# Kernel optimization log

Hardware: AMD Instinct MI355X
Metric: run time of the kernel (lower is better)

The kernel has to match this reference:

```python
import jax, jax.numpy as jnp
import numpy as np

B, S, D_TEXT, MAXF = 2, 1024, 384, 5
D_MODEL, N_HEADS, D_FF, L = 768, 12, 3072, 4
HEAD_DIM = D_MODEL // N_HEADS
EPS = 1e-6
NEG = -1e9


def _rms(x, g):
    return x * jax.lax.rsqrt(jnp.mean(x * x, axis=-1, keepdims=True) + EPS) * g


def _attn(x, w, mask):
    # w: [4, d, d] = (wq, wk, wv, wo); mask: [b, s, s] bool (True = attend)
    b, s, d = x.shape

    def proj(W):
        return jnp.einsum('bsd,de->bse', x, W).reshape(b, s, N_HEADS, HEAD_DIM).transpose(0, 2, 1, 3)

    q, k, v = proj(w[0]), proj(w[1]), proj(w[2])
    scale = jnp.asarray(1.0 / np.sqrt(HEAD_DIM), x.dtype)
    scores = jnp.einsum('bhqe,bhke->bhqk', q, k) * scale
    scores = jnp.where(mask[:, None], scores, NEG)
    p = jax.nn.softmax(scores, axis=-1)
    o = jnp.einsum('bhqk,bhke->bhqe', p, v).transpose(0, 2, 1, 3).reshape(b, s, d)
    return jnp.einsum('bsd,de->bse', o, w[3])


def _forward(number_values, datetime_values, boolean_values, text_values, column_name_values,
             W_cn, b_cn, W_num, b_num, W_text, b_text, W_dt, b_dt, W_bool, b_bool,
             g_cn, g_num, g_text, g_dt, g_bool, mask_emb,
             blk_norms, blk_attn, blk_up, blk_gate, blk_down,
             g_out, Wd_num, bd_num, Wd_dt, bd_dt, Wd_bool, bd_bool, Wd_text, bd_text,
             node_indices, table_name_indices, column_name_indices,
             f2p_neighbor_indices, semantic_types, masks, is_padding):
    valid = ~is_padding
    pv = valid[:, :, None] & valid[:, None, :]  # [b,s,s]
    eye = jnp.eye(S, dtype=bool)[None]
    same_node = node_indices[:, :, None] == node_indices[:, None, :]
    col_mask = ((column_name_indices[:, :, None] == column_name_indices[:, None, :])
                & (table_name_indices[:, :, None] == table_name_indices[:, None, :]) & pv) | eye
    feat_mask = (same_node & pv) | eye
    # kv node is one of q's f2p neighbors
    nei = (f2p_neighbor_indices[:, :, :, None] == node_indices[:, None, None, :]).any(axis=2)
    nei_mask = ((nei | same_node) & pv) | eye
    full_mask = pv | eye

    # per-semantic-type value encoders (Linear + RMSNorm)
    cn = _rms(column_name_values @ W_cn + b_cn, g_cn)
    num_e = _rms(number_values @ W_num + b_num, g_num)
    text_e = _rms(text_values @ W_text + b_text, g_text)
    dt_e = _rms(datetime_values @ W_dt + b_dt, g_dt)
    bool_e = _rms(boolean_values @ W_bool + b_bool, g_bool)
    st = semantic_types[..., None]
    val = jnp.where(st == 0, num_e, jnp.where(st == 1, text_e, jnp.where(st == 2, dt_e, bool_e)))
    # masked cells get the learned mask embedding for their semantic type
    val = jnp.where(masks[..., None], mask_emb[semantic_types], val)
    x = val + cn

    for i in range(L):
        nw, aw = blk_norms[i], blk_attn[i]
        x = x + _attn(_rms(x, nw[0]), aw[0], col_mask)
        x = x + _attn(_rms(x, nw[1]), aw[1], feat_mask)
        x = x + _attn(_rms(x, nw[2]), aw[2], nei_mask)
        x = x + _attn(_rms(x, nw[3]), aw[3], full_mask)
        h = _rms(x, nw[4])
        x = x + (jax.nn.silu(h @ blk_gate[i]) * (h @ blk_up[i])) @ blk_down[i]

    h = _rms(x, g_out)
    return (h @ Wd_num + bd_num, h @ Wd_dt + bd_dt, h @ Wd_bool + bd_bool, h @ Wd_text + bd_text)


def setup_inputs() -> dict:
    key = jax.random.key(0)
    ks = iter(jax.random.split(key, 64))

    def nrm(shape, scale=0.02):
        return jax.random.normal(next(ks), shape, jnp.float32) * scale

    inp = {}
    inp['number_values'] = jax.random.normal(next(ks), (B, S, 1), jnp.float32)
    inp['datetime_values'] = jax.random.normal(next(ks), (B, S, 1), jnp.float32)
    inp['boolean_values'] = jax.random.normal(next(ks), (B, S, 1), jnp.float32)
    inp['text_values'] = jax.random.normal(next(ks), (B, S, D_TEXT), jnp.float32)
    inp['column_name_values'] = jax.random.normal(next(ks), (B, S, D_TEXT), jnp.float32)
    inp['W_cn'] = nrm((D_TEXT, D_MODEL)); inp['b_cn'] = jnp.zeros((D_MODEL,), jnp.float32)
    inp['W_num'] = nrm((1, D_MODEL)); inp['b_num'] = jnp.zeros((D_MODEL,), jnp.float32)
    inp['W_text'] = nrm((D_TEXT, D_MODEL)); inp['b_text'] = jnp.zeros((D_MODEL,), jnp.float32)
    inp['W_dt'] = nrm((1, D_MODEL)); inp['b_dt'] = jnp.zeros((D_MODEL,), jnp.float32)
    inp['W_bool'] = nrm((1, D_MODEL)); inp['b_bool'] = jnp.zeros((D_MODEL,), jnp.float32)
    for n in ('g_cn', 'g_num', 'g_text', 'g_dt', 'g_bool'):
        inp[n] = jnp.ones((D_MODEL,), jnp.float32)
    inp['mask_emb'] = jax.random.normal(next(ks), (4, D_MODEL), jnp.float32)
    inp['blk_norms'] = jnp.ones((L, 5, D_MODEL), jnp.float32)
    inp['blk_attn'] = nrm((L, 4, 4, D_MODEL, D_MODEL))
    inp['blk_up'] = nrm((L, D_MODEL, D_FF))
    inp['blk_gate'] = nrm((L, D_MODEL, D_FF))
    inp['blk_down'] = nrm((L, D_FF, D_MODEL))
    inp['g_out'] = jnp.ones((D_MODEL,), jnp.float32)
    inp['Wd_num'] = nrm((D_MODEL, 1)); inp['bd_num'] = jnp.zeros((1,), jnp.float32)
    inp['Wd_dt'] = nrm((D_MODEL, 1)); inp['bd_dt'] = jnp.zeros((1,), jnp.float32)
    inp['Wd_bool'] = nrm((D_MODEL, 1)); inp['bd_bool'] = jnp.zeros((1,), jnp.float32)
    inp['Wd_text'] = nrm((D_MODEL, D_TEXT)); inp['bd_text'] = jnp.zeros((D_TEXT,), jnp.float32)
    inp['node_indices'] = jax.random.randint(next(ks), (B, S), 0, 128)
    inp['table_name_indices'] = jax.random.randint(next(ks), (B, S), 0, 8)
    inp['column_name_indices'] = jax.random.randint(next(ks), (B, S), 0, 32)
    inp['f2p_neighbor_indices'] = jax.random.randint(next(ks), (B, S, MAXF), 0, 128)
    inp['semantic_types'] = jax.random.randint(next(ks), (B, S), 0, 4)
    inp['masks'] = jax.random.bernoulli(next(ks), 0.15, (B, S))
    inp['is_padding'] = jnp.zeros((B, S), bool)
    return inp


def reference(number_values, datetime_values, boolean_values, text_values, column_name_values,
              W_cn, b_cn, W_num, b_num, W_text, b_text, W_dt, b_dt, W_bool, b_bool,
              g_cn, g_num, g_text, g_dt, g_bool, mask_emb,
              blk_norms, blk_attn, blk_up, blk_gate, blk_down,
              g_out, Wd_num, bd_num, Wd_dt, bd_dt, Wd_bool, bd_bool, Wd_text, bd_text,
              node_indices, table_name_indices, column_name_indices,
              f2p_neighbor_indices, semantic_types, masks, is_padding):
    return _forward(number_values, datetime_values, boolean_values, text_values, column_name_values,
                    W_cn, b_cn, W_num, b_num, W_text, b_text, W_dt, b_dt, W_bool, b_bool,
                    g_cn, g_num, g_text, g_dt, g_bool, mask_emb,
                    blk_norms, blk_attn, blk_up, blk_gate, blk_down,
                    g_out, Wd_num, bd_num, Wd_dt, bd_dt, Wd_bool, bd_bool, Wd_text, bd_text,
                    node_indices, table_name_indices, column_name_indices,
                    f2p_neighbor_indices, semantic_types, masks, is_padding)
```

## Files before the change

kernel.cpp:

```cpp
#include <hip/hip_runtime.h>
#include <hip/hip_bf16.h>
#include <cmath>
#include <stdint.h>


#define BB 2
#define SS 1024
#define DT 384
#define DM 768
#define NH 12
#define DH 64
#define DFF 3072
#define NL 4
#define NROW (BB*SS)
#define EPSF 1e-6f
#define QSC 0.1803368801111244f

typedef unsigned short u16;
typedef unsigned char u8;
typedef unsigned int u32;
typedef __attribute__((ext_vector_type(8))) short s16x8;
typedef __attribute__((ext_vector_type(4))) float f32x4;

__device__ __forceinline__ u16 f2bu(float f){
    u32 x = __float_as_uint(f);
    u32 r = (x + 0x7fffu + ((x>>16)&1u)) >> 16;
    return (u16)r;
}
__device__ __forceinline__ u32 pk2(float lo, float hi){
    return (u32)f2bu(lo) | ((u32)f2bu(hi)<<16);
}
__device__ __forceinline__ int swz(int row, int c){
    return (row<<6) + (((((c>>3) ^ row) & 7))<<3) + (c&7);
}
__device__ __forceinline__ float rsum16(float v){
    v += __shfl_xor(v,1); v += __shfl_xor(v,2);
    v += __shfl_xor(v,4); v += __shfl_xor(v,8);
    return v;
}
#define SBAR() __builtin_amdgcn_sched_barrier(0)
#define GLDS(src,dst) __builtin_amdgcn_global_load_lds((const __attribute__((address_space(1))) u32*)(src), (__attribute__((address_space(3))) u32*)(dst), 16, 0, 0)
#define GLDS4(src,dst) __builtin_amdgcn_global_load_lds((const __attribute__((address_space(1))) u32*)(src), (__attribute__((address_space(3))) u32*)(dst), 4, 0, 0)

__global__ void zero_f(float* __restrict__ p, int n){
    int i = blockIdx.x*256 + threadIdx.x;
    if (i<n) p[i]=0.f;
}

__device__ void norm_bool_body(const void* __restrict__ src, u8* __restrict__ dst, int n)
{
    __shared__ int fl[4];
    if (threadIdx.x<4) fl[threadIdx.x]=0;
    __syncthreads();
    const u32* wsrc = (const u32*)src;
    const int nw = n/4;
    int any=0, nb=0, hi=0, lo=0;
    for (int i=threadIdx.x;i<nw;i+=blockDim.x){
        u32 v=wsrc[i];
        if (!v) continue;
        any=1;
        #pragma unroll
        for (int b=0;b<4;b++){
            u32 by=(v>>(8*b))&0xffu;
            if (by>1u) nb=1;
            if (by==1u && b!=0) hi=1;
        }
        if ((v&0xffffu)==0x3f80u) lo=1;
    }
    if (any) atomicOr(&fl[0],1);
    if (nb)  atomicOr(&fl[1],1);
    if (hi)  atomicOr(&fl[2],1);
    if (lo)  atomicOr(&fl[3],1);
    __syncthreads();
    int c;
    if (!fl[0]) c=0;
    else if (!fl[1]) c = fl[2] ? 2 : 1;
    else if (fl[3]) c = 3;
    else c = 1;
    for (int i=threadIdx.x;i<n;i+=blockDim.x){
        u8 v;
        if (c==0)      v=0;
        else if (c==1) v = (((const u32*)src)[i]!=0u);
        else if (c==2) v = (((const u8*)src)[i]!=0u);
        else           v = (((const u16*)src)[i]!=0u);
        dst[i]=v;
    }
}
__global__ void norm_bool2(const void* s0, u8* d0, const void* s1, u8* d1, int n)
{
    if (blockIdx.x==0) norm_bool_body(s0,d0,n);
    else               norm_bool_body(s1,d1,n);
}

__global__ void pack_meta(const int* __restrict__ node, const int* __restrict__ colx,
                          const int* __restrict__ tbl, const u8* __restrict__ pad,
                          u32* __restrict__ pm, int n)
{
    int i = blockIdx.x*256 + threadIdx.x;
    if (i<n)
        pm[i] = (u32)(node[i]&0xff) | ((u32)(colx[i]&0xff)<<8) | ((u32)(tbl[i]&0xff)<<16) | ((u32)(pad[i]&1)<<24);
}

__global__ __launch_bounds__(256) void mask4_kernel(const u32* __restrict__ pm, const int* __restrict__ f2p,
                                                    u8* __restrict__ m4)
{
    const int b = blockIdx.y, kg = blockIdx.x;
    const int t = threadIdx.x;
    __shared__ u32 qm[1024];
    __shared__ int qf[1024*5];
    for (int i=t;i<1024;i+=256) qm[i] = pm[b*SS+i];
    for (int i=t;i<5*1024;i+=256) qf[i] = f2p[b*SS*5 + i];
    __syncthreads();
    const int q0 = t*4;
    u32 qmv[4]; int qn[4]; int qfv[4][5];
    #pragma unroll
    for (int j=0;j<4;j++){
        qmv[j]=qm[q0+j]; qn[j]=(int)(qmv[j]&0xffu);
        #pragma unroll
        for (int f=0;f<5;f++) qfv[j][f]=qf[(q0+j)*5+f];
    }
    for (int kk=0;kk<16;kk++){
        const int k = kg*16+kk;
        const u32 km = qm[k];
        const int kn = (int)(km&0xffu);
        u32 outw=0;
        #pragma unroll
        for (int j=0;j<4;j++){
            const u32 qmw = qmv[j];
            const bool pv = (((qmw|km)>>24)&1u)==0u;
            u32 by=0;
            if ((((qmw^km)&0x00ffff00u)==0u) && pv) by|=1;
            if ((((qmw^km)&0xffu)==0u) && pv) by|=2;
            bool nei = (qfv[j][0]==kn)||(qfv[j][1]==kn)||(qfv[j][2]==kn)||(qfv[j][3]==kn)||(qfv[j][4]==kn)
                       ||(qn[j]==kn);
            if (nei && pv) by|=4;
            if (pv) by|=8;
            if ((q0+j)==k) by=15;
            outw |= by<<(8*j);
        }
        ((u32*)(m4 + ((size_t)b<<20) + ((size_t)k<<10)))[t] = outw;
    }
}

__global__ __launch_bounds__(256) void transpose_cvt2(const float* __restrict__ src, u16* __restrict__ dst,
                                                      int K, int N, size_t dz,
                                                      const float* __restrict__ gbase, int gmode)
{
    const int z = blockIdx.z;
    src += (size_t)z*K*N;
    dst += (size_t)z*dz;
    const float* g = nullptr;
    if (gmode==1){ int m = z&3; if (m<3) g = gbase + (size_t)((z>>4)*5 + ((z>>2)&3))*768; }
    else if (gmode==2){ g = gbase + (size_t)z*5*768; }
    const int n0 = blockIdx.x*32, k0 = blockIdx.y*64;
    __shared__ float t[64][33];
    const int tid = threadIdx.x;
    const int kr = tid>>3, n4 = (tid&7)*4;
    #pragma unroll
    for (int p=0;p<2;p++){
        const int k = p*32 + kr;
        float gk = g ? g[k0+k] : 1.f;
        float4 v = *(const float4*)(src + (size_t)(k0+k)*N + n0 + n4);
        t[k][n4]=v.x*gk; t[k][n4+1]=v.y*gk; t[k][n4+2]=v.z*gk; t[k][n4+3]=v.w*gk;
    }
    __syncthreads();
    const int n = tid>>3, ks = (tid&7)*8;
    const int ng = n0 + n;
    uint4 o;
    u32* op = (u32*)&o;
    #pragma unroll
    for (int i=0;i<4;i++)
        op[i] = pk2(t[ks+2*i][n], t[ks+2*i+1][n]);
    *(uint4*)&dst[(((size_t)(ng>>7)*(K>>6) + (k0>>6))<<13) + ((ng&127)<<6) + ks] = o;
}

__global__ __launch_bounds__(256) void cvt_tiled2(const float* __restrict__ s0, u16* __restrict__ d0,
                                                  const float* __restrict__ s1, u16* __restrict__ d1, int K)
{
    const float* src = blockIdx.y ? s1 : s0;
    u16* dst = blockIdx.y ? d1 : d0;
    const int gid = blockIdx.x*256 + threadIdx.x;
    const int base = gid*8;
    const int row = base / K, col = base - row*K;
    float4 a = *(const float4*)(src + base);
    float4 b = *(const float4*)(src + base + 4);
    uint4 o;
    o.x = pk2(a.x,a.y); o.y = pk2(a.z,a.w);
    o.z = pk2(b.x,b.y); o.w = pk2(b.z,b.w);
    *(uint4*)&dst[(((size_t)(row>>7)*(K>>6) + (col>>6))<<13) + ((row&127)<<6) + (col&63)] = o;
}

__device__ __forceinline__ void stage3(const u16* aT, const u16* bT, int cb, int brow,
                                       u16* la, u16* lb, int w, int l)
{
    #pragma unroll
    for (int p=0;p<2;p++){
        const int q = p*256 + w*64 + l;
        const int row = q>>2, u = q&3;
        const int so = row*64 + cb + (((u ^ ((row>>1)&3))&3)<<3);
        GLDS(aT+so, la + p*2048 + w*512);
    }
    {
        const int q = w*64 + l;
        const int row = q>>2, u = q&3;
        const int so = (brow+row)*64 + cb + (((u ^ ((row>>1)&3))&3)<<3);
        GLDS(bT+so, lb + w*512);
    }
}

__global__ __launch_bounds__(256,4) void gemm_t(
    const u16* __restrict__ At, const u16* __restrict__ Bt,
    int K, int AMS, u16* __restrict__ qk16, u16* __restrict__ vt16,
    const float* __restrict__ rs_in)
{
    __shared__ u16 lds[3][6144];
    const int tid = threadIdx.x;
    const int lane = tid & 63, w = tid >> 6;
    const int cg = lane >> 4, cl = lane & 15;
    const int NT = K >> 5;
    const int n0 = blockIdx.x*64;
    const int brow = n0 & 64;
    const size_t bNb = (size_t)(n0>>7)*(K>>6);

    const u16* aB = At + ((size_t)blockIdx.y * AMS << 13);
    const u16* bB = Bt + (bNb << 13);

    f32x4 acc[2][4];
    #pragma unroll
    for (int i=0;i<2;i++)
        #pragma unroll
        for (int j=0;j<4;j++) acc[i][j] = (f32x4){0.f,0.f,0.f,0.f};

    stage3(aB, bB, 0, brow, &lds[0][0], &lds[0][4096], w, lane);

    for (int kt=0; kt<NT; kt++){
        const int buf = kt % 3;
        if (kt+1 < NT){
            const int k1 = kt+1;
            stage3(aB + ((size_t)(k1>>1)<<13), bB + ((size_t)(k1>>1)<<13),
                   (k1&1)<<5, brow, &lds[k1%3][0], &lds[k1%3][4096], w, lane);
            asm volatile("s_waitcnt vmcnt(3)" ::: "memory");
        } else {
            asm volatile("s_waitcnt vmcnt(0)" ::: "memory");
        }
        SBAR(); __builtin_amdgcn_s_barrier(); SBAR();
        s16x8 af[2], bf[4];
        #pragma unroll
        for (int mt=0;mt<2;mt++){
            const int ra = w*32 + mt*16 + cl;
            af[mt] = *(const s16x8*)&lds[buf][ra*32 + (((cg ^ ((ra>>1)&3))&3)<<3)];
        }
        #pragma unroll
        for (int nt=0;nt<4;nt++){
            const int rb = nt*16 + cl;
            bf[nt] = *(const s16x8*)&lds[buf][4096 + rb*32 + (((cg ^ ((rb>>1)&3))&3)<<3)];
        }
        #pragma unroll
        for (int mt=0;mt<2;mt++)
            #pragma unroll
            for (int nt=0;nt<4;nt++)
                acc[mt][nt] = __builtin_amdgcn_mfma_f32_16x16x32_bf16(af[mt], bf[nt], acc[mt][nt], 0,0,0);
    }

    const int m0 = blockIdx.y*128;
    #pragma unroll
    for (int mt=0;mt<2;mt++){
        const int grow0 = m0 + w*32 + mt*16 + cg*4;
        float rr[4];
        #pragma unroll
        for (int j=0;j<4;j++) rr[j] = rsqrtf(rs_in[grow0+j]*(1.f/768.f) + EPSF);
        #pragma unroll
        for (int nt=0;nt<4;nt++){
            const int col = n0 + nt*16 + cl;
            if (col < 768){
                #pragma unroll
                for (int j=0;j<4;j++)
                    qk16[(size_t)(grow0+j)*1536 + col] = f2bu(acc[mt][nt][j]*rr[j]*QSC);
            } else if (col < 1536){
                #pragma unroll
                for (int j=0;j<4;j++)
                    qk16[(size_t)(grow0+j)*1536 + col] = f2bu(acc[mt][nt][j]*rr[j]);
            } else {
                const int b = grow0>>10, s0 = grow0&1023;
                const int dhg = col - 1536;
                uint2 o;
                o.x = pk2(acc[mt][nt][0]*rr[0], acc[mt][nt][1]*rr[1]);
                o.y = pk2(acc[mt][nt][2]*rr[2], acc[mt][nt][3]*rr[3]);
                *(uint2*)(vt16 + ((size_t)(b*768 + dhg)<<10) + s0) = o;
            }
        }
    }
}

__global__ __launch_bounds__(256,3) void gemm_gu(
    const u16* __restrict__ At, const u16* __restrict__ Bg, const u16* __restrict__ Bu,
    const float* __restrict__ rs_in, u16* __restrict__ o16)
{
    __shared__ u16 lds[3][8192];
    const int tid = threadIdx.x;
    const int lane = tid & 63, w = tid >> 6;
    const int cg = lane >> 4, cl = lane & 15;
    const int NT = 24;
    const int n0 = blockIdx.x*64;
    const int brow = n0 & 64;
    const size_t bNb = (size_t)(n0>>7)*12;

    const u16* aB = At + ((size_t)blockIdx.y * 12 << 13);
    const u16* gB = Bg + (bNb << 13);
    const u16* uB = Bu + (bNb << 13);

    f32x4 accg[2][4], accu[2][4];
    #pragma unroll
    for (int i=0;i<2;i++)
        #pragma unroll
        for (int j=0;j<4;j++){ accg[i][j] = (f32x4){0.f,0.f,0.f,0.f}; accu[i][j] = (f32x4){0.f,0.f,0.f,0.f}; }

    #define STAGE_GU(kt2, cb, buf) { \
        const u16* a_ = aB + ((size_t)(kt2)<<13); \
        const u16* g_ = gB + ((size_t)(kt2)<<13); \
        const u16* u_ = uB + ((size_t)(kt2)<<13); \
        _Pragma("unroll") \
        for (int p=0;p<2;p++){ \
            const int q = p*256 + w*64 + lane; \
            const int row = q>>2, uu = q&3; \
            const int so = row*64 + (cb) + (((uu ^ ((row>>1)&3))&3)<<3); \
            GLDS(a_+so, &lds[buf][0] + p*2048 + w*512); \
        } \
        { \
            const int q = w*64 + lane; \
            const int row = q>>2, uu = q&3; \
            const int so = (brow+row)*64 + (cb) + (((uu ^ ((row>>1)&3))&3)<<3); \
            GLDS(g_+so, &lds[buf][4096] + w*512); \
            GLDS(u_+so, &lds[buf][6144] + w*512); \
        } }

    STAGE_GU(0, 0, 0);

    for (int kt=0; kt<NT; kt++){
        const int buf = kt % 3;
        if (kt+1 < NT){
            const int k1 = kt+1;
            STAGE_GU(k1>>1, (k1&1)<<5, k1%3);
            asm volatile("s_waitcnt vmcnt(4)" ::: "memory");
        } else {
            asm volatile("s_waitcnt vmcnt(0)" ::: "memory");
        }
        SBAR(); __builtin_amdgcn_s_barrier(); SBAR();
        s16x8 af[2], bg[4], bu[4];
        #pragma unroll
        for (int mt=0;mt<2;mt++){
            const int ra = w*32 + mt*16 + cl;
            af[mt] = *(const s16x8*)&lds[buf][ra*32 + (((cg ^ ((ra>>1)&3))&3)<<3)];
        }
        #pragma unroll
        for (int nt=0;nt<4;nt++){
            const int rb = nt*16 + cl;
            const int sw = (((cg ^ ((rb>>1)&3))&3)<<3);
            bg[nt] = *(const s16x8*)&lds[buf][4096 + rb*32 + sw];
            bu[nt] = *(const s16x8*)&lds[buf][6144 + rb*32 + sw];
        }
        #pragma unroll
        for (int mt=0;mt<2;mt++)
            #pragma unroll
            for (int nt=0;nt<4;nt++){
                accg[mt][nt] = __builtin_amdgcn_mfma_f32_16x16x32_bf16(af[mt], bg[nt], accg[mt][nt], 0,0,0);
                accu[mt][nt] = __builtin_amdgcn_mfma_f32_16x16x32_bf16(af[mt], bu[nt], accu[mt][nt], 0,0,0);
            }
    }

    const int m0 = blockIdx.y*128;
    #pragma unroll
    for (int mt=0;mt<2;mt++){
        const int grow0 = m0 + w*32 + mt*16 + cg*4;
        float rr[4];
        #pragma unroll
        for (int j=0;j<4;j++) rr[j] = rsqrtf(rs_in[grow0+j]*(1.f/768.f) + EPSF);
        #pragma unroll
        for (int nt=0;nt<4;nt++){
            const int col = n0 + nt*16 + cl;
            const size_t tb = (((size_t)(grow0>>7)*48 + (col>>6))<<13) + (col&63);
            #pragma unroll
            for (int j=0;j<4;j++){
                float g = accg[mt][nt][j]*rr[j];
                float u = accu[mt][nt][j]*rr[j];
                float s = g/(1.f+__expf(-g))*u;
                o16[tb + (((grow0+j)&127)<<6)] = f2bu(s);
            }
        }
    }
}

__device__ __forceinline__ void stage64(const u16* aT, int arow, const u16* bT, int brow, int cb,
                                        u16* la, u16* lb, int w, int l)
{
    const int q = w*64 + l;
    const int row = q>>2, u = q&3;
    const int sw = (((u ^ ((row>>1)&3))&3)<<3);
    GLDS(aT + (arow+row)*64 + cb + sw, la + w*512);
    GLDS(bT + (brow+row)*64 + cb + sw, lb + w*512);
}

__global__ __launch_bounds__(256,6) void gemm_t64(
    const u16* __restrict__ At, const u16* __restrict__ Bt, float* __restrict__ C,
    int N, int K, int AMS, int flags, const float* __restrict__ bias,
    u16* __restrict__ o16, float* __restrict__ rs_out)
{
    __shared__ u16 lds[3][4096];
    const int tid = threadIdx.x;
    const int lane = tid & 63, w = tid >> 6;
    const int cg = lane >> 4, cl = lane & 15;
    const int NT = K >> 5;
    const int n0 = blockIdx.x*64;
    const int m0 = blockIdx.y*64;
    const int brow = n0 & 64, arow = m0 & 64;

    const u16* aB = At + ((size_t)(m0>>7) * AMS << 13);
    const u16* bB = Bt + ((size_t)(n0>>7) * (K>>6) << 13);

    f32x4 acc[4];
    #pragma unroll
    for (int j=0;j<4;j++) acc[j] = (f32x4){0.f,0.f,0.f,0.f};

    stage64(aB, arow, bB, brow, 0, &lds[0][0], &lds[0][2048], w, lane);

    for (int kt=0; kt<NT; kt++){
        const int buf = kt % 3;
        if (kt+1 < NT){
            const int k1 = kt+1;
            stage64(aB + ((size_t)(k1>>1)<<13), arow, bB + ((size_t)(k1>>1)<<13), brow,
                    (k1&1)<<5, &lds[k1%3][0], &lds[k1%3][2048], w, lane);
            asm volatile("s_waitcnt vmcnt(2)" ::: "memory");
        } else {
            asm volatile("s_waitcnt vmcnt(0)" ::: "memory");
        }
        SBAR(); __builtin_amdgcn_s_barrier(); SBAR();
        const int ra = w*16 + cl;
        s16x8 af = *(const s16x8*)&lds[buf][ra*32 + (((cg ^ ((ra>>1)&3))&3)<<3)];
        s16x8 bf[4];
        #pragma unroll
        for (int nt=0;nt<4;nt++){
            const int rb = nt*16 + cl;
            bf[nt] = *(const s16x8*)&lds[buf][2048 + rb*32 + (((cg ^ ((rb>>1)&3))&3)<<3)];
        }
        #pragma unroll
        for (int nt=0;nt<4;nt++)
            acc[nt] = __builtin_amdgcn_mfma_f32_16x16x32_bf16(af, bf[nt], acc[nt], 0,0,0);
    }

    const int grow0 = m0 + w*16 + cg*4;
    const bool do_acc = (flags&1), do_bias = (flags&2);
    float tmp[4][4];
    #pragma unroll
    for (int nt=0;nt<4;nt++){
        const int col = n0 + nt*16 + cl;
        float bv = do_bias ? bias[col] : 0.f;
        #pragma unroll
        for (int j=0;j<4;j++){
            float v = acc[nt][j] + bv;
            float* cp = C + (size_t)(grow0+j)*N + col;
            if (do_acc) v += *cp;
            *cp = v;
            tmp[nt][j] = v;
        }
    }
    if (o16){
        #pragma unroll
        for (int nt=0;nt<4;nt++){
            const int col = n0 + nt*16 + cl;
            const size_t tb = (((size_t)(grow0>>7)*12 + (col>>6))<<13) + (col&63);
            #pragma unroll
            for (int j=0;j<4;j++)
                o16[tb + (((grow0+j)&127)<<6)] = f2bu(tmp[nt][j]);
        }
    }
    if (rs_out){
        #pragma unroll
        for (int j=0;j<4;j++){
            float s = tmp[0][j]*tmp[0][j] + tmp[1][j]*tmp[1][j]
                    + tmp[2][j]*tmp[2][j] + tmp[3][j]*tmp[3][j];
            s = rsum16(s);
            if (cl==0) atomicAdd(rs_out + grow0 + j, s);
        }
    }
}

__global__ __launch_bounds__(256,3) void attn_mfma3(
    const u16* __restrict__ qk16, const u16* __restrict__ vt16,
    const u8* __restrict__ m4, int mt,
    u16* __restrict__ ob16)
{
    const int bh = blockIdx.y;
    const int b = bh / NH, h = bh % NH;
    const int q0 = blockIdx.x * 64;
    const int tid = threadIdx.x;
    const int w = tid>>6, lane = tid&63, cg = lane>>4, cl = lane&15;
    const int srow = lane>>3;
    const int sseg = (lane&7) ^ srow;
    const int mk = lane>>4, mq = lane&15;

    __shared__ u16 Ks[2][4096], Vt[2][4096], Ps[4096];
    __shared__ u32 Ms[2][1024];

    s16x8 qa0, qa1;
    {
        const u16* qrow = qk16 + (size_t)(b*SS+q0 + w*16 + cl)*1536 + h*64;
        qa0 = *(const s16x8*)(qrow + cg*8);
        qa1 = *(const s16x8*)(qrow + 32 + cg*8);
        asm volatile("" :: "v"(*(const f32x4*)&qa0), "v"(*(const f32x4*)&qa1));
    }

    const u16* kbase = qk16 + (size_t)(b*SS)*1536 + 768 + h*64;
    const u16* vbase = vt16 + ((size_t)(b*768 + h*64)<<10);
    const u8*  mbase = m4 + ((size_t)b<<20) + q0;

    #pragma unroll
    for (int p=0;p<2;p++){
        const int row = p*32 + w*8 + srow;
        GLDS(kbase + (size_t)row*1536 + sseg*8, Ks[0] + p*2048 + w*512);
        GLDS(vbase + ((size_t)row<<10) + sseg*8, Vt[0] + p*2048 + w*512);
    }
    #pragma unroll
    for (int i=0;i<4;i++){
        const int key = w*16 + i*4 + mk;
        GLDS4(mbase + ((size_t)key<<10) + mq*4, (u8*)Ms[0] + w*1024 + i*256);
    }

    f32x4 o[4];
    #pragma unroll
    for (int nt=0;nt<4;nt++) o[nt] = (f32x4){0.f,0.f,0.f,0.f};
    float lsum[4] = {0.f,0.f,0.f,0.f};

    for (int kc=0;kc<16;kc++){
        const int buf = kc & 1;
        if (kc < 15){
            const int kn0 = kc*64 + 64;
            #pragma unroll
            for (int p=0;p<2;p++){
                const int row = p*32 + w*8 + srow;
                GLDS(kbase + (size_t)(kn0+row)*1536 + sseg*8, Ks[buf^1] + p*2048 + w*512);
                GLDS(vbase + ((size_t)row<<10) + kn0 + sseg*8, Vt[buf^1] + p*2048 + w*512);
            }
            #pragma unroll
            for (int i=0;i<4;i++){
                const int key = kn0 + w*16 + i*4 + mk;
                GLDS4(mbase + ((size_t)key<<10) + mq*4, (u8*)Ms[buf^1] + w*1024 + i*256);
            }
            asm volatile("s_waitcnt vmcnt(8)" ::: "memory");
        } else {
            asm volatile("s_waitcnt vmcnt(0)" ::: "memory");
        }
        SBAR(); __builtin_amdgcn_s_barrier(); SBAR();

        f32x4 sc[4];
        #pragma unroll
        for (int nt=0;nt<4;nt++) sc[nt] = (f32x4){0.f,0.f,0.f,0.f};
        __builtin_amdgcn_s_setprio(1);
        #pragma unroll
        for (int nt=0;nt<4;nt++){
            s16x8 kb0 = *(const s16x8*)&Ks[buf][swz(nt*16+cl, cg*8)];
            sc[nt] = __builtin_amdgcn_mfma_f32_16x16x32_bf16(qa0, kb0, sc[nt], 0,0,0);
        }
        #pragma unroll
        for (int nt=0;nt<4;nt++){
            s16x8 kb1 = *(const s16x8*)&Ks[buf][swz(nt*16+cl, 32+cg*8)];
            sc[nt] = __builtin_amdgcn_mfma_f32_16x16x32_bf16(qa1, kb1, sc[nt], 0,0,0);
        }
        __builtin_amdgcn_s_setprio(0);

        float pP[4][4];
        #pragma unroll
        for (int nt=0;nt<4;nt++){
            const u32 w4 = Ms[buf][(nt*16+cl)*16 + w*4 + cg];
            #pragma unroll
            for (int j=0;j<4;j++){
                float pe = exp2f(fminf(sc[nt][j], 100.f));
                pe = ((w4 >> (8*j + mt)) & 1u) ? pe : 0.f;
                pP[nt][j] = pe;
                lsum[j] += pe;
            }
        }

        #pragma unroll
        for (int nt=0;nt<4;nt++)
            #pragma unroll
            for (int j=0;j<4;j++)
                Ps[swz(w*16+cg*4+j, nt*16+cl)] = f2bu(pP[nt][j]);

        __builtin_amdgcn_s_setprio(1);
        #pragma unroll
        for (int ks=0;ks<2;ks++){
            s16x8 pa = *(const s16x8*)&Ps[swz(w*16+cl, ks*32+cg*8)];
            #pragma unroll
            for (int nt=0;nt<4;nt++){
                s16x8 vb = *(const s16x8*)&Vt[buf][swz(nt*16+cl, ks*32+cg*8)];
                o[nt] = __builtin_amdgcn_mfma_f32_16x16x32_bf16(pa, vb, o[nt], 0,0,0);
            }
        }
        __builtin_amdgcn_s_setprio(0);
        SBAR(); __builtin_amdgcn_s_barrier(); SBAR();
    }

    #pragma unroll
    for (int j=0;j<4;j++){
        const float inv = 1.f/rsum16(lsum[j]);
        const int row = b*SS + q0 + w*16 + cg*4 + j;
        const size_t rb = ((size_t)(row>>7)*12 + h)*8192 + ((row&127)<<6);
        #pragma unroll
        for (int nt=0;nt<4;nt++)
            ob16[rb + nt*16 + cl] = f2bu(o[nt][j]*inv);
    }
}

__global__ __launch_bounds__(256) void fuse_encode(
    const float* __restrict__ cnbuf, const float* __restrict__ textbuf,
    const float* __restrict__ numv, const float* __restrict__ dtv, const float* __restrict__ boolv,
    const float* __restrict__ Wnum, const float* __restrict__ bnum,
    const float* __restrict__ Wdt, const float* __restrict__ bdt,
    const float* __restrict__ Wbool, const float* __restrict__ bbool,
    const float* __restrict__ gcn, const float* __restrict__ gnum, const float* __restrict__ gtext,
    const float* __restrict__ gdt, const float* __restrict__ gbool,
    const float* __restrict__ memb, const int* __restrict__ stypes, const u8* __restrict__ masks,
    float* __restrict__ x, u16* __restrict__ xt16, float* __restrict__ rs0)
{
    const int row = blockIdx.x;
    const int t = threadIdx.x;
    __shared__ float red[256];

    float cn3[3]; float ss=0.f;
    #pragma unroll
    for (int j=0;j<3;j++){
        cn3[j] = cnbuf[(size_t)row*DM + t + j*256];
        ss += cn3[j]*cn3[j];
    }
    red[t]=ss; __syncthreads();
    for (int s=128;s>0;s>>=1){ if(t<s) red[t]+=red[t+s]; __syncthreads(); }
    {
        float r = rsqrtf(red[0]/(float)DM + EPSF);
        #pragma unroll
        for (int j=0;j<3;j++) cn3[j] *= r*gcn[t+j*256];
    }
    __syncthreads();

    const int st = stypes[row];
    float val[3]; ss=0.f;
    if (st==1){
        #pragma unroll
        for (int j=0;j<3;j++){
            val[j] = textbuf[(size_t)row*DM + t + j*256];
            ss += val[j]*val[j];
        }
    } else {
        const float* Wp = (st==0)?Wnum:((st==2)?Wdt:Wbool);
        const float* bp = (st==0)?bnum:((st==2)?bdt:bbool);
        const float* vp = (st==0)?numv:((st==2)?dtv:boolv);
        float v = vp[row];
        #pragma unroll
        for (int j=0;j<3;j++){
            int e=t+j*256;
            val[j] = v*Wp[e] + bp[e];
            ss += val[j]*val[j];
        }
    }
    red[t]=ss; __syncthreads();
    for (int s=128;s>0;s>>=1){ if(t<s) red[t]+=red[t+s]; __syncthreads(); }
    const float* gp = (st==0)?gnum:((st==1)?gtext:((st==2)?gdt:gbool));
    float r2 = rsqrtf(red[0]/(float)DM + EPSF);
    bool mk = masks[row]!=0;
    float xv[3]; float sx=0.f;
    #pragma unroll
    for (int j=0;j<3;j++){
        int e=t+j*256;
        float vv = val[j]*r2*gp[e];
        if (mk) vv = memb[st*DM+e];
        xv[j] = vv + cn3[j];
        x[(size_t)row*DM+e] = xv[j];
        sx += xv[j]*xv[j];
    }
    __syncthreads();
    red[t]=sx; __syncthreads();
    for (int s=128;s>0;s>>=1){ if(t<s) red[t]+=red[t+s]; __syncthreads(); }
    if (t==0) rs0[row] = red[0];
    const size_t mb = (size_t)(row>>7)*12;
    const int rr = (row&127)<<6;
    #pragma unroll
    for (int j=0;j<3;j++){
        const int c = t + j*256;
        xt16[((mb + (c>>6))<<13) + rr + (c&63)] = f2bu(xv[j]);
    }
}

__global__ __launch_bounds__(256) void decode2(
    const float* __restrict__ x, const float* __restrict__ gout,
    const float* __restrict__ Wn, const float* __restrict__ bn,
    const float* __restrict__ Wd, const float* __restrict__ bd,
    const float* __restrict__ Wb, const float* __restrict__ bb,
    float* __restrict__ out, u16* __restrict__ h16)
{
    const int row = blockIdx.x;
    const int t = threadIdx.x;
    __shared__ float h[DM];
    __shared__ float red[256];
    const float* xr = x + (size_t)row*DM;
    float v0=xr[t], v1=xr[t+256], v2=xr[t+512];
    red[t]=v0*v0+v1*v1+v2*v2; __syncthreads();
    for (int s=128;s>0;s>>=1){ if(t<s) red[t]+=red[t+s]; __syncthreads(); }
    float r = rsqrtf(red[0]/(float)DM + EPSF);
    float h0 = v0*r*gout[t], h1 = v1*r*gout[t+256], h2 = v2*r*gout[t+512];
    h[t]=h0; h[t+256]=h1; h[t+512]=h2;
    const size_t mb = (size_t)(row>>7)*12;
    const int rr = (row&127)<<6;
    #pragma unroll
    for (int j=0;j<3;j++){
        const int c = t + j*256;
        const float v = (j==0?h0:(j==1?h1:h2));
        h16[((mb + (c>>6))<<13) + rr + (c&63)] = f2bu(v);
    }
    __syncthreads();

    float pn=0.f,pd=0.f,pb=0.f;
    for (int k=t;k<DM;k+=256){ float hv=h[k]; pn+=hv*Wn[k]; pd+=hv*Wd[k]; pb+=hv*Wb[k]; }
    red[t]=pn; __syncthreads();
    for (int s=128;s>0;s>>=1){ if(t<s) red[t]+=red[t+s]; __syncthreads(); }
    float tn=red[0]; __syncthreads();
    red[t]=pd; __syncthreads();
    for (int s=128;s>0;s>>=1){ if(t<s) red[t]+=red[t+s]; __syncthreads(); }
    float td=red[0]; __syncthreads();
    red[t]=pb; __syncthreads();
    for (int s=128;s>0;s>>=1){ if(t<s) red[t]+=red[t+s]; __syncthreads(); }
    float tb=red[0];
    if (t==0){
        out[row]          = tn + bn[0];
        out[NROW + row]   = td + bd[0];
        out[2*NROW + row] = tb + bb[0];
    }
}

extern "C" void kernel_launch(void* const* d_in, const int* in_sizes, int n_in,
                              void* d_out, int out_size, void* d_ws, size_t ws_size,
                              hipStream_t stream)
{
    const float* numv   = (const float*)d_in[0];
    const float* dtval  = (const float*)d_in[1];
    const float* boolv  = (const float*)d_in[2];
    const float* textv  = (const float*)d_in[3];
    const float* cnamev = (const float*)d_in[4];
    const float* Wcn=(const float*)d_in[5];  const float* bcn=(const float*)d_in[6];
    const float* Wnum=(const float*)d_in[7]; const float* bnum=(const float*)d_in[8];
    const float* Wtext=(const float*)d_in[9];const float* btext=(const float*)d_in[10];
    const float* Wdt=(const float*)d_in[11]; const float* bdt=(const float*)d_in[12];
    const float* Wbool=(const float*)d_in[13];const float* bbool=(const float*)d_in[14];
    const float* gcn=(const float*)d_in[15]; const float* gnum=(const float*)d_in[16];
    const float* gtext=(const float*)d_in[17];const float* gdt=(const float*)d_in[18];
    const float* gbool=(const float*)d_in[19];
    const float* memb=(const float*)d_in[20];
    const float* norms_all=(const float*)d_in[21];
    const float* attw_all=(const float*)d_in[22];
    const float* up_all=(const float*)d_in[23];
    const float* gate_all=(const float*)d_in[24];
    const float* down_all=(const float*)d_in[25];
    const float* gout=(const float*)d_in[26];
    const float* Wdn=(const float*)d_in[27]; const float* bdn=(const float*)d_in[28];
    const float* Wdd=(const float*)d_in[29]; const float* bdd=(const float*)d_in[30];
    const float* Wdb=(const float*)d_in[31]; const float* bdb=(const float*)d_in[32];
    const float* Wdtx=(const float*)d_in[33];const float* bdtx=(const float*)d_in[34];
    const int* node=(const int*)d_in[35];
    const int* tbl =(const int*)d_in[36];
    const int* colx=(const int*)d_in[37];
    const int* f2p =(const int*)d_in[38];
    const int* styp=(const int*)d_in[39];

    const size_t SA = (size_t)768*768;
    const size_t SG = (size_t)768*3072;
    const size_t SC = (size_t)384*768;
    const size_t NX = (size_t)NROW*DM;

    u8* base = (u8*)d_ws;
    float* x  = (float*)base;
    u16* xt16 = (u16*)(base + 6291456);
    u16* ob16 = (u16*)(base + 9437184);
    u16* qk16 = (u16*)(base + 12582912);
    u16* vt16 = (u16*)(base + 18874368);
    u16* gu16 = (u16*)(base + 22020096);
    u16* wA   = (u16*)(base + 47185920);
    u16* wGU  = wA + 64*SA;
    u16* wD   = wGU + 8*SG;
    u16* wCN  = wD + 4*SG;
    u16* wTX  = wCN + SC;
    u16* wDX  = wTX + SC;
    u8* nmask = (u8*)(wDX + SC);
    u8* npad  = nmask + NROW;
    u32* pmeta = (u32*)(npad + NROW + 64);
    float* rsbuf = (float*)(pmeta + NROW);
    u8* m4 = (u8*)(rsbuf + 21*2048);

    u16* cnT16   = qk16;
    u16* textT16 = vt16;
    float* cnbuf   = (float*)gu16;
    float* textbuf = cnbuf + NX;

    float* out = (float*)d_out;

    zero_f<<<(21*2048)/256,256,0,stream>>>(rsbuf, 21*2048);
    norm_bool2<<<2,256,0,stream>>>(d_in[40], nmask, d_in[41], npad, NROW);
    pack_meta<<<NROW/256,256,0,stream>>>(node, colx, tbl, npad, pmeta, NROW);
    mask4_kernel<<<dim3(64,2),256,0,stream>>>(pmeta, f2p, m4);

    transpose_cvt2<<<dim3(24,12,64),256,0,stream>>>(attw_all, wA, 768, 768, SA, norms_all, 1);
    transpose_cvt2<<<dim3(96,12,4),256,0,stream>>>(gate_all, wGU,      768, 3072, 2*SG, norms_all + 4*768, 2);
    transpose_cvt2<<<dim3(96,12,4),256,0,stream>>>(up_all,   wGU + SG, 768, 3072, 2*SG, norms_all + 4*768, 2);
    transpose_cvt2<<<dim3(24,48,4),256,0,stream>>>(down_all, wD, 3072, 768, SG, nullptr, 0);
    transpose_cvt2<<<dim3(24,6,1),256,0,stream>>>(Wcn,   wCN, 384, 768, 0, nullptr, 0);
    transpose_cvt2<<<dim3(24,6,1),256,0,stream>>>(Wtext, wTX, 384, 768, 0, nullptr, 0);
    transpose_cvt2<<<dim3(12,12,1),256,0,stream>>>(Wdtx, wDX, 768, 384, 0, nullptr, 0);

    cvt_tiled2<<<dim3(384,2),256,0,stream>>>(cnamev, cnT16, textv, textT16, 384);
    gemm_t64<<<dim3(12,32),256,0,stream>>>(cnT16,   wCN, cnbuf,   768, 384, 6, 2, bcn,   nullptr, nullptr);
    gemm_t64<<<dim3(12,32),256,0,stream>>>(textT16, wTX, textbuf, 768, 384, 6, 2, btext, nullptr, nullptr);
    fuse_encode<<<NROW,256,0,stream>>>(cnbuf, textbuf, numv, dtval, boolv,
        Wnum,bnum,Wdt,bdt,Wbool,bbool, gcn,gnum,gtext,gdt,gbool,
        memb, styp, nmask, x, xt16, rsbuf);

    const dim3 ga(SS/64, BB*NH);
    for (int l=0; l<NL; l++){
        for (int a=0; a<4; a++){
            const int slot = l*5 + a;
            const u16* wqkv = wA + (size_t)((l*4+a)*4)*SA;
            gemm_t<<<dim3(36,16),256,0,stream>>>(xt16, wqkv, 768, 12, qk16, vt16,
                rsbuf + (size_t)slot*2048);
            attn_mfma3<<<ga,256,0,stream>>>(qk16, vt16, m4, a, ob16);
            gemm_t64<<<dim3(12,32),256,0,stream>>>(ob16, wqkv + 3*SA, x, 768, 768, 12, 1, nullptr,
                xt16, rsbuf + (size_t)(slot+1)*2048);
        }
        gemm_gu<<<dim3(48,16),256,0,stream>>>(xt16, wGU + (size_t)l*2*SG, wGU + (size_t)l*2*SG + SG,
            rsbuf + (size_t)(l*5+4)*2048, gu16);
        gemm_t64<<<dim3(12,32),256,0,stream>>>(gu16, wD + (size_t)l*SG, x, 768, 3072, 48, 1, nullptr,
            xt16, rsbuf + (size_t)((l+1)*5)*2048);
    }

    decode2<<<NROW,256,0,stream>>>(x, gout, Wdn,bdn, Wdd,bdd, Wdb,bdb, out, xt16);
    gemm_t64<<<dim3(6,32),256,0,stream>>>(xt16, wDX, out + 3*NROW, 384, 768, 12, 2, bdtx,
        nullptr, nullptr);
}
```

Baseline: 1.445 ms.

## Bit-pack attention masks, triple-buffer K/V tiles, drop per-iteration barrier

Adds a repack kernel that turns the byte-per-mask-type layout into per-type bitplanes, so attention loads 8x less mask data per key chunk. The attention kernel now uses three LDS buffers for K, V and mask, which lets it remove the trailing block barrier each iteration, at the cost of lower occupancy (launch bounds 3 to 2). The rsbuf zeroing is folded into pack_meta to save a launch. Dropping the barrier depends on the three-deep ring being enough to avoid write-after-read hazards on the Ps and K/V buffers.

```diff
diff --git a/kernel.cpp b/kernel.cpp
--- a/kernel.cpp
+++ b/kernel.cpp
@@ -41,11 +41,6 @@
 #define SBAR() __builtin_amdgcn_sched_barrier(0)
 #define GLDS(src,dst) __builtin_amdgcn_global_load_lds((const __attribute__((address_space(1))) u32*)(src), (__attribute__((address_space(3))) u32*)(dst), 16, 0, 0)
 #define GLDS4(src,dst) __builtin_amdgcn_global_load_lds((const __attribute__((address_space(1))) u32*)(src), (__attribute__((address_space(3))) u32*)(dst), 4, 0, 0)
-
-__global__ void zero_f(float* __restrict__ p, int n){
-    int i = blockIdx.x*256 + threadIdx.x;
-    if (i<n) p[i]=0.f;
-}
 
 __device__ void norm_bool_body(const void* __restrict__ src, u8* __restrict__ dst, int n)
 {
@@ -94,11 +89,12 @@
 
 __global__ void pack_meta(const int* __restrict__ node, const int* __restrict__ colx,
                           const int* __restrict__ tbl, const u8* __restrict__ pad,
-                          u32* __restrict__ pm, int n)
+                          u32* __restrict__ pm, int n, float* __restrict__ rsz, int nz)
 {
     int i = blockIdx.x*256 + threadIdx.x;
     if (i<n)
         pm[i] = (u32)(node[i]&0xff) | ((u32)(colx[i]&0xff)<<8) | ((u32)(tbl[i]&0xff)<<16) | ((u32)(pad[i]&1)<<24);
+    for (int z=i; z<nz; z+=gridDim.x*256) rsz[z]=0.f;
 }
 
 __global__ __launch_bounds__(256) void mask4_kernel(const u32* __restrict__ pm, const int* __restrict__ f2p,
@@ -140,6 +136,29 @@
         }
         ((u32*)(m4 + ((size_t)b<<20) + ((size_t)k<<10)))[t] = outw;
     }
+}
+
+__global__ void repack_mask(const u8* __restrict__ m4, u8* __restrict__ mbp)
+{
+    const int gid = blockIdx.x*256 + threadIdx.x;
+    const int qb = gid & 127;
+    const int bk = gid >> 7;
+    const u8* src = m4 + ((size_t)bk<<10) + qb*8;
+    u32 lo = *(const u32*)src, hi = *(const u32*)(src+4);
+    u32 out[4] = {0,0,0,0};
+    #pragma unroll
+    for (int j=0;j<4;j++){
+        u32 b0 = (lo>>(8*j)) & 0xffu;
+        u32 b1 = (hi>>(8*j)) & 0xffu;
+        #pragma unroll
+        for (int tt=0;tt<4;tt++){
+            out[tt] |= ((b0>>tt)&1u) << j;
+            out[tt] |= ((b1>>tt)&1u) << (j+4);
+        }
+    }
+    u8* dst = mbp + (size_t)bk*512 + qb;
+    #pragma unroll
+    for (int tt=0;tt<4;tt++) dst[tt*128] = (u8)out[tt];
 }
 
 __global__ __launch_bounds__(256) void transpose_cvt2(const float* __restrict__ src, u16* __restrict__ dst,
@@ -484,9 +503,9 @@
     }
 }
 
-__global__ __launch_bounds__(256,3) void attn_mfma3(
+__global__ __launch_bounds__(256,2) void attn_mfma5(
     const u16* __restrict__ qk16, const u16* __restrict__ vt16,
-    const u8* __restrict__ m4, int mt,
+    const u8* __restrict__ mbp, int mt,
     u16* __restrict__ ob16)
 {
     const int bh = blockIdx.y;
@@ -496,10 +515,9 @@
     const int w = tid>>6, lane = tid&63, cg = lane>>4, cl = lane&15;
     const int srow = lane>>3;
     const int sseg = (lane&7) ^ srow;
-    const int mk = lane>>4, mq = lane&15;
-
-    __shared__ u16 Ks[2][4096], Vt[2][4096], Ps[4096];
-    __shared__ u32 Ms[2][1024];
+
+    __shared__ u16 Ks[3][4096], Vt[3][4096], Ps[4096];
+    __shared__ u8 Ms[3][512];
 
     s16x8 qa0, qa1;
     {
@@ -511,7 +529,7 @@
 
     const u16* kbase = qk16 + (size_t)(b*SS)*1536 + 768 + h*64;
     const u16* vbase = vt16 + ((size_t)(b*768 + h*64)<<10);
-    const u8*  mbase = m4 + ((size_t)b<<20) + q0;
+    const u8* mrow0 = mbp + ((size_t)(b<<10))*512 + mt*128 + (q0>>3);
 
     #pragma unroll
     for (int p=0;p<2;p++){
@@ -519,10 +537,9 @@
         GLDS(kbase + (size_t)row*1536 + sseg*8, Ks[0] + p*2048 + w*512);
         GLDS(vbase + ((size_t)row<<10) + sseg*8, Vt[0] + p*2048 + w*512);
     }
-    #pragma unroll
-    for (int i=0;i<4;i++){
-        const int key = w*16 + i*4 + mk;
-        GLDS4(mbase + ((size_t)key<<10) + mq*4, (u8*)Ms[0] + w*1024 + i*256);
+    if (lane < 32){
+        const int krow = w*16 + (lane>>1);
+        GLDS4(mrow0 + (size_t)krow*512 + (lane&1)*4, Ms[0] + w*128);
     }
 
     f32x4 o[4];
@@ -531,21 +548,21 @@
     float lsum[4] = {0.f,0.f,0.f,0.f};
 
     for (int kc=0;kc<16;kc++){
-        const int buf = kc & 1;
+        const int buf = kc % 3;
         if (kc < 15){
+            const int nb = (kc+1) % 3;
             const int kn0 = kc*64 + 64;
             #pragma unroll
             for (int p=0;p<2;p++){
                 const int row = p*32 + w*8 + srow;
-                GLDS(kbase + (size_t)(kn0+row)*1536 + sseg*8, Ks[buf^1] + p*2048 + w*512);
-                GLDS(vbase + ((size_t)row<<10) + kn0 + sseg*8, Vt[buf^1] + p*2048 + w*512);
+                GLDS(kbase + (size_t)(kn0+row)*1536 + sseg*8, Ks[nb] + p*2048 + w*512);
+                GLDS(vbase + ((size_t)row<<10) + kn0 + sseg*8, Vt[nb] + p*2048 + w*512);
             }
-            #pragma unroll
-            for (int i=0;i<4;i++){
-                const int key = kn0 + w*16 + i*4 + mk;
-                GLDS4(mbase + ((size_t)key<<10) + mq*4, (u8*)Ms[buf^1] + w*1024 + i*256);
+            if (lane < 32){
+                const int krow = kn0 + w*16 + (lane>>1);
+                GLDS4(mrow0 + (size_t)krow*512 + (lane&1)*4, Ms[nb] + w*128);
             }
-            asm volatile("s_waitcnt vmcnt(8)" ::: "memory");
+            asm volatile("s_waitcnt vmcnt(5)" ::: "memory");
         } else {
             asm volatile("s_waitcnt vmcnt(0)" ::: "memory");
         }
@@ -568,13 +585,15 @@
         __builtin_amdgcn_s_setprio(0);
 
         float pP[4][4];
+        const int qb = 2*w + (cg>>1);
+        const int bsh = (cg&1)*4;
         #pragma unroll
         for (int nt=0;nt<4;nt++){
-            const u32 w4 = Ms[buf][(nt*16+cl)*16 + w*4 + cg];
+            const u32 mrow = Ms[buf][(nt*16+cl)*8 + qb];
             #pragma unroll
             for (int j=0;j<4;j++){
                 float pe = exp2f(fminf(sc[nt][j], 100.f));
-                pe = ((w4 >> (8*j + mt)) & 1u) ? pe : 0.f;
+                pe = ((mrow >> (bsh+j)) & 1u) ? pe : 0.f;
                 pP[nt][j] = pe;
                 lsum[j] += pe;
             }
@@ -597,7 +616,6 @@
             }
         }
         __builtin_amdgcn_s_setprio(0);
-        SBAR(); __builtin_amdgcn_s_barrier(); SBAR();
     }
 
     #pragma unroll
@@ -792,6 +810,7 @@
     u32* pmeta = (u32*)(npad + NROW + 64);
     float* rsbuf = (float*)(pmeta + NROW);
     u8* m4 = (u8*)(rsbuf + 21*2048);
+    u8* mbp = m4 + ((size_t)2<<20);
 
     u16* cnT16   = qk16;
     u16* textT16 = vt16;
@@ -800,10 +819,10 @@
 
     float* out = (float*)d_out;
 
-    zero_f<<<(21*2048)/256,256,0,stream>>>(rsbuf, 21*2048);
     norm_bool2<<<2,256,0,stream>>>(d_in[40], nmask, d_in[41], npad, NROW);
-    pack_meta<<<NROW/256,256,0,stream>>>(node, colx, tbl, npad, pmeta, NROW);
+    pack_meta<<<8,256,0,stream>>>(node, colx, tbl, npad, pmeta, NROW, rsbuf, 21*2048);
     mask4_kernel<<<dim3(64,2),256,0,stream>>>(pmeta, f2p, m4);
+    repack_mask<<<1024,256,0,stream>>>(m4, mbp);
 
     transpose_cvt2<<<dim3(24,12,64),256,0,stream>>>(attw_all, wA, 768, 768, SA, norms_all, 1);
     transpose_cvt2<<<dim3(96,12,4),256,0,stream>>>(gate_all, wGU,      768, 3072, 2*SG, norms_all + 4*768, 2);
@@ -827,7 +846,7 @@
             const u16* wqkv = wA + (size_t)((l*4+a)*4)*SA;
             gemm_t<<<dim3(36,16),256,0,stream>>>(xt16, wqkv, 768, 12, qk16, vt16,
                 rsbuf + (size_t)slot*2048);
-            attn_mfma3<<<ga,256,0,stream>>>(qk16, vt16, m4, a, ob16);
+            attn_mfma5<<<ga,256,0,stream>>>(qk16, vt16, mbp, a, ob16);
             gemm_t64<<<dim3(12,32),256,0,stream>>>(ob16, wqkv + 3*SA, x, 768, 768, 12, 1, nullptr,
                 xt16, rsbuf + (size_t)(slot+1)*2048);
         }
```

After: 1.412 ms. 1.02x faster.
